# Performance work log

Hardware: AMD Instinct MI355X
Metric: run time of the kernel (lower is better)

## Reference

```python
import jax, jax.numpy as jnp
import numpy as np

N_NODES = 50000
N_EDGES = 800000
F = 64
R = 32


def setup_inputs() -> dict:
    key = jax.random.key(0)
    ks = jax.random.split(key, 12)
    s = jax.random.normal(ks[0], (N_NODES, F), dtype=jnp.float32)
    v = jax.random.normal(ks[1], (N_NODES, 3, F), dtype=jnp.float32)
    radial_embeddings = jax.random.normal(ks[2], (N_EDGES, R), dtype=jnp.float32)
    f_cut = jax.random.uniform(ks[3], (N_EDGES,), dtype=jnp.float32)
    unit_vectors = jax.random.normal(ks[4], (N_EDGES, 3), dtype=jnp.float32)
    edge_index = jax.random.randint(ks[5], (2, N_EDGES), 0, N_NODES, dtype=jnp.int64 if jax.config.jax_enable_x64 else jnp.int32)
    # mlp_phi: Linear(F,F) -> SiLU -> Linear(F, 3F); linear_W: Linear(R, 3F)
    W1 = jax.random.normal(ks[6], (F, F), dtype=jnp.float32) / np.sqrt(F)
    b1 = jnp.zeros((F,), dtype=jnp.float32)
    W2 = jax.random.normal(ks[7], (F, 3 * F), dtype=jnp.float32) / np.sqrt(F)
    b2 = jnp.zeros((3 * F,), dtype=jnp.float32)
    Wr = jax.random.normal(ks[8], (R, 3 * F), dtype=jnp.float32) / np.sqrt(R)
    br = jnp.zeros((3 * F,), dtype=jnp.float32)
    return {"s": s, "v": v, "radial_embeddings": radial_embeddings, "f_cut": f_cut,
            "unit_vectors": unit_vectors, "edge_index": edge_index,
            "W1": W1, "b1": b1, "W2": W2, "b2": b2, "Wr": Wr, "br": br}


def reference(s, v, radial_embeddings, f_cut, unit_vectors, edge_index, W1, b1, W2, b2, Wr, br):
    idx_i, idx_j = edge_index[0], edge_index[1]
    n_nodes = s.shape[0]
    nf = s.shape[-1]
    # per-node MLP: Linear -> SiLU -> Linear to 3F channels
    phi = jax.nn.silu(s @ W1 + b1) @ W2 + b2            # [N, 3F]
    # radial filter weighted by cutoff
    W = (radial_embeddings @ Wr + br) * f_cut[:, None]   # [E, 3F]
    x = phi[idx_j] * W                                   # [E, 3F]  (gather + multiply)
    x_s, x_vv, x_vs = x[:, :nf], x[:, nf:2 * nf], x[:, 2 * nf:]
    ds = jax.ops.segment_sum(x_s, idx_i, num_segments=n_nodes)          # [N, F]
    x_v = v[idx_j] * x_vv[:, None, :] + x_vs[:, None, :] * unit_vectors[:, :, None]  # [E, 3, F]
    dv = jax.ops.segment_sum(x_v, idx_i, num_segments=n_nodes)          # [N, 3, F]
    return s + ds, v + dv
```

## Files before the change

### kernel.cpp

```cpp
#include <hip/hip_runtime.h>
#include <math.h>

#define N_NODES 50000
#define N_EDGES 800000
#define F 64
#define R 32
#define C3F 192
#define CAP 48
#define CSTRIDE 16
#define MLP_BLOCKS ((N_NODES + 31) / 32)
#define FILL_BLOCKS ((N_EDGES + 1023) / 1024)

#define REP32(X) X(0) X(1) X(2) X(3) X(4) X(5) X(6) X(7) \
                 X(8) X(9) X(10) X(11) X(12) X(13) X(14) X(15) \
                 X(16) X(17) X(18) X(19) X(20) X(21) X(22) X(23) \
                 X(24) X(25) X(26) X(27) X(28) X(29) X(30) X(31)

__device__ __forceinline__ float bcastf(float x, int l) {
    return __uint_as_float((unsigned)__builtin_amdgcn_readlane(
        (int)__float_as_uint(x), l));
}

__global__ __launch_bounds__(256) void mlp_fill_kernel(
    const float* __restrict__ s, const float* __restrict__ W1,
    const float* __restrict__ b1, const float* __restrict__ W2,
    const float* __restrict__ b2, float* __restrict__ phi,
    const int* __restrict__ eidx, int* __restrict__ counts,
    int2* __restrict__ bucket)
{
    __shared__ float hid_s[32][68];

    if (blockIdx.x >= MLP_BLOCKS) {
        int base = (blockIdx.x - MLP_BLOCKS) * 1024 + threadIdx.x;
        int ii[4], jj[4];
#pragma unroll
        for (int q = 0; q < 4; q++) {
            int e = base + q * 256;
            ii[q] = -1;
            if (e < N_EDGES) {
                ii[q] = __builtin_nontemporal_load(&eidx[e]);
                jj[q] = __builtin_nontemporal_load(&eidx[N_EDGES + e]);
            }
        }
#pragma unroll
        for (int q = 0; q < 4; q++) {
            int e = base + q * 256;
            if (ii[q] >= 0) {
                int pos = atomicAdd(&counts[ii[q] * CSTRIDE], 1);
                if (pos < CAP)
                    bucket[(size_t)ii[q] * CAP + pos] = make_int2(e, jj[q]);
            }
        }
        return;
    }

    int n = threadIdx.x >> 3;
    int seg = threadIdx.x & 7;
    int node = blockIdx.x * 32 + n;
    bool live = node < N_NODES;

    if (live) {
        float sv[F];
        const float4* srow = (const float4*)(s + (size_t)node * F);
#pragma unroll
        for (int q = 0; q < F / 4; q++) {
            float4 t = srow[q];
            sv[4*q+0] = t.x; sv[4*q+1] = t.y; sv[4*q+2] = t.z; sv[4*q+3] = t.w;
        }
        float acc[8];
#pragma unroll
        for (int q = 0; q < 8; q++) acc[q] = b1[seg * 8 + q];
#pragma unroll
        for (int k = 0; k < F; k++) {
            float sk = sv[k];
            const float4* w = (const float4*)(W1 + (size_t)k * F + seg * 8);
            float4 w0 = w[0], w1 = w[1];
            acc[0] += sk * w0.x; acc[1] += sk * w0.y;
            acc[2] += sk * w0.z; acc[3] += sk * w0.w;
            acc[4] += sk * w1.x; acc[5] += sk * w1.y;
            acc[6] += sk * w1.z; acc[7] += sk * w1.w;
        }
#pragma unroll
        for (int q = 0; q < 8; q++) {
            float a = acc[q];
            hid_s[n][seg * 8 + q] = a / (1.f + __expf(-a));
        }
    }
    __syncthreads();

    if (!live) return;

    float hv[F];
#pragma unroll
    for (int q = 0; q < F; q++) hv[q] = hid_s[n][q];

    float acc[24];
#pragma unroll
    for (int q = 0; q < 24; q++) acc[q] = b2[seg * 24 + q];
#pragma unroll
    for (int k = 0; k < F; k++) {
        float hk = hv[k];
        const float4* w = (const float4*)(W2 + (size_t)k * C3F + seg * 24);
#pragma unroll
        for (int q4 = 0; q4 < 6; q4++) {
            float4 wv = w[q4];
            acc[q4*4+0] += hk * wv.x;
            acc[q4*4+1] += hk * wv.y;
            acc[q4*4+2] += hk * wv.z;
            acc[q4*4+3] += hk * wv.w;
        }
    }
    float4* o = (float4*)(phi + (size_t)node * C3F + seg * 24);
#pragma unroll
    for (int q4 = 0; q4 < 6; q4++)
        o[q4] = make_float4(acc[q4*4+0], acc[q4*4+1], acc[q4*4+2], acc[q4*4+3]);
}

__global__ __launch_bounds__(64, 3) void gather_kernel(
    const float* __restrict__ s, const float* __restrict__ v,
    const float* __restrict__ phi, const float* __restrict__ radial,
    const float* __restrict__ f_cut, const float* __restrict__ unit_vec,
    const float* __restrict__ Wr, const float* __restrict__ br,
    const int* __restrict__ counts, const int2* __restrict__ bucket,
    float* __restrict__ out_s, float* __restrict__ out_v)
{
    const int lane = threadIdx.x;
    const int node = blockIdx.x;

#define DECL_WR(r) float wrs##r, wrv##r, wrq##r;
    REP32(DECL_WR)
#undef DECL_WR
#define LOAD_WR(r) { const float* w_ = Wr + (r) * C3F; \
                     wrs##r = w_[lane]; wrv##r = w_[64 + lane]; \
                     wrq##r = w_[128 + lane]; }
    REP32(LOAD_WR)
#undef LOAD_WR

#define KA3(r) , "+v"(wrs##r), "+v"(wrv##r), "+v"(wrq##r)
#define PIN_WR \
    asm volatile("" : "+v"(wrs0) KA3(1) KA3(2) KA3(3) KA3(4) KA3(5) KA3(6) KA3(7), "+v"(wrv0), "+v"(wrq0)); \
    asm volatile("" : "+v"(wrs8) KA3(9) KA3(10) KA3(11) KA3(12) KA3(13) KA3(14) KA3(15), "+v"(wrv8), "+v"(wrq8)); \
    asm volatile("" : "+v"(wrs16) KA3(17) KA3(18) KA3(19) KA3(20) KA3(21) KA3(22) KA3(23), "+v"(wrv16), "+v"(wrq16)); \
    asm volatile("" : "+v"(wrs24) KA3(25) KA3(26) KA3(27) KA3(28) KA3(29) KA3(30) KA3(31), "+v"(wrv24), "+v"(wrq24));
    PIN_WR

    const float b_s = br[lane], b_vv = br[64 + lane], b_vs = br[128 + lane];

    float acc_s = 0.f, acc_v0 = 0.f, acc_v1 = 0.f, acc_v2 = 0.f;

    int cnt = __builtin_amdgcn_readfirstlane(counts[node * CSTRIDE]);
    cnt = cnt < CAP ? cnt : CAP;

    const int* rowi = (const int*)(bucket + (size_t)node * CAP);
    int ejx = 0, ejy = 0;
    if (lane < cnt) {
        ejx = __builtin_nontemporal_load(rowi + 2 * lane);
        ejy = __builtin_nontemporal_load(rowi + 2 * lane + 1);
    }
    float fcL = __builtin_nontemporal_load(&f_cut[ejx]);
    float u0L = __builtin_nontemporal_load(&unit_vec[ejx * 3 + 0]);
    float u1L = __builtin_nontemporal_load(&unit_vec[ejx * 3 + 1]);
    float u2L = __builtin_nontemporal_load(&unit_vec[ejx * 3 + 2]);

    if (cnt > 0) {
        int e = __builtin_amdgcn_readlane(ejx, 0);
        int j = __builtin_amdgcn_readlane(ejy, 0);
        const float* pj = phi + (size_t)j * C3F;
        const float* vj = v + (size_t)j * C3F;
        float ps = pj[lane], pvv = pj[64 + lane], pvs = pj[128 + lane];
        float va = vj[lane], vb = vj[64 + lane], vc = vj[128 + lane];
        float rl = __builtin_nontemporal_load(
            &radial[(size_t)(unsigned)e * R + (lane & 31)]);

        for (int k = 0; k < cnt; ++k) {
            int kn = (k + 1 < cnt) ? k + 1 : k;
            int j_n = __builtin_amdgcn_readlane(ejy, kn);
            int e_n = __builtin_amdgcn_readlane(ejx, kn);
            const float* pn = phi + (size_t)(unsigned)j_n * C3F;
            const float* vn = v + (size_t)(unsigned)j_n * C3F;
            float nps = pn[lane], npvv = pn[64 + lane], npvs = pn[128 + lane];
            float nva = vn[lane], nvb = vn[64 + lane], nvc = vn[128 + lane];
            float nrl = __builtin_nontemporal_load(
                &radial[(size_t)(unsigned)e_n * R + (lane & 31)]);

            float fc = bcastf(fcL, k);
            float u0 = bcastf(u0L, k);
            float u1 = bcastf(u1L, k);
            float u2 = bcastf(u2L, k);

            PIN_WR

            float ws = b_s, wvv = b_vv, wvs = b_vs;
#define FMA_WR(r) { float rr = bcastf(rl, r); ws += rr * wrs##r; \
                    wvv += rr * wrv##r; wvs += rr * wrq##r; }
            REP32(FMA_WR)
#undef FMA_WR

            float xs  = ps  * ws  * fc;
            float xvv = pvv * wvv * fc;
            float xvs = pvs * wvs * fc;
            acc_s  += xs;
            acc_v0 += va * xvv + xvs * u0;
            acc_v1 += vb * xvv + xvs * u1;
            acc_v2 += vc * xvv + xvs * u2;

            e = e_n; j = j_n;
            ps = nps; pvv = npvv; pvs = npvs;
            va = nva; vb = nvb; vc = nvc;
            rl = nrl;
        }
    }
#undef KA3
#undef PIN_WR

    float so = s[(size_t)node * F + lane] + acc_s;
    __builtin_nontemporal_store(so, &out_s[(size_t)node * F + lane]);
    const float* vi = v + (size_t)node * C3F;
    float* ovi = out_v + (size_t)node * C3F;
    __builtin_nontemporal_store(vi[lane]       + acc_v0, &ovi[lane]);
    __builtin_nontemporal_store(vi[64 + lane]  + acc_v1, &ovi[64 + lane]);
    __builtin_nontemporal_store(vi[128 + lane] + acc_v2, &ovi[128 + lane]);
}

extern "C" void kernel_launch(void* const* d_in, const int* in_sizes, int n_in,
                              void* d_out, int out_size, void* d_ws, size_t ws_size,
                              hipStream_t stream)
{
    const float* s      = (const float*)d_in[0];
    const float* v      = (const float*)d_in[1];
    const float* radial = (const float*)d_in[2];
    const float* f_cut  = (const float*)d_in[3];
    const float* unit   = (const float*)d_in[4];
    const int*   eidx   = (const int*)  d_in[5];
    const float* W1     = (const float*)d_in[6];
    const float* b1     = (const float*)d_in[7];
    const float* W2     = (const float*)d_in[8];
    const float* b2     = (const float*)d_in[9];
    const float* Wr     = (const float*)d_in[10];
    const float* br     = (const float*)d_in[11];

    float* out   = (float*)d_out;
    float* out_s = out;
    float* out_v = out + (size_t)N_NODES * F;

    float* phi    = (float*)d_ws;
    int*   counts = (int*)(phi + (size_t)N_NODES * C3F);
    int2*  bucket = (int2*)(counts + (size_t)N_NODES * CSTRIDE);

    hipMemsetAsync(counts, 0, (size_t)N_NODES * CSTRIDE * sizeof(int), stream);

    mlp_fill_kernel<<<MLP_BLOCKS + FILL_BLOCKS, 256, 0, stream>>>(
        s, W1, b1, W2, b2, phi, eidx, counts, bucket);

    gather_kernel<<<N_NODES, 64, 0, stream>>>(
        s, v, phi, radial, f_cut, unit, Wr, br,
        counts, bucket, out_s, out_v);
}
```

Measured before the change: 605.5 us.

## Double-buffer edge loads two ahead and use scalar radial loads

The gather loop now keeps two in-flight edge buffers (A/B), so phi, v and radial data are prefetched two edges ahead instead of one. Radial embeddings are read as 32 uniform scalar loads per edge instead of a per-lane load plus readlane broadcasts. The occupancy hint rises from 3 to 4 waves. The extra buffer adds about 38 live registers against the tighter launch bound, which could cause spills.

```diff
diff --git a/kernel.cpp b/kernel.cpp
--- a/kernel.cpp
+++ b/kernel.cpp
@@ -116,7 +116,7 @@
         o[q4] = make_float4(acc[q4*4+0], acc[q4*4+1], acc[q4*4+2], acc[q4*4+3]);
 }
 
-__global__ __launch_bounds__(64, 3) void gather_kernel(
+__global__ __launch_bounds__(64, 4) void gather_kernel(
     const float* __restrict__ s, const float* __restrict__ v,
     const float* __restrict__ phi, const float* __restrict__ radial,
     const float* __restrict__ f_cut, const float* __restrict__ unit_vec,
@@ -163,52 +163,81 @@
     float u2L = __builtin_nontemporal_load(&unit_vec[ejx * 3 + 2]);
 
     if (cnt > 0) {
-        int e = __builtin_amdgcn_readlane(ejx, 0);
-        int j = __builtin_amdgcn_readlane(ejy, 0);
-        const float* pj = phi + (size_t)j * C3F;
-        const float* vj = v + (size_t)j * C3F;
-        float ps = pj[lane], pvv = pj[64 + lane], pvs = pj[128 + lane];
-        float va = vj[lane], vb = vj[64 + lane], vc = vj[128 + lane];
-        float rl = __builtin_nontemporal_load(
-            &radial[(size_t)(unsigned)e * R + (lane & 31)]);
-
-        for (int k = 0; k < cnt; ++k) {
-            int kn = (k + 1 < cnt) ? k + 1 : k;
-            int j_n = __builtin_amdgcn_readlane(ejy, kn);
-            int e_n = __builtin_amdgcn_readlane(ejx, kn);
-            const float* pn = phi + (size_t)(unsigned)j_n * C3F;
-            const float* vn = v + (size_t)(unsigned)j_n * C3F;
-            float nps = pn[lane], npvv = pn[64 + lane], npvs = pn[128 + lane];
-            float nva = vn[lane], nvb = vn[64 + lane], nvc = vn[128 + lane];
-            float nrl = __builtin_nontemporal_load(
-                &radial[(size_t)(unsigned)e_n * R + (lane & 31)]);
-
-            float fc = bcastf(fcL, k);
-            float u0 = bcastf(u0L, k);
-            float u1 = bcastf(u1L, k);
-            float u2 = bcastf(u2L, k);
-
-            PIN_WR
-
-            float ws = b_s, wvv = b_vv, wvs = b_vs;
-#define FMA_WR(r) { float rr = bcastf(rl, r); ws += rr * wrs##r; \
-                    wvv += rr * wrv##r; wvs += rr * wrq##r; }
-            REP32(FMA_WR)
-#undef FMA_WR
-
-            float xs  = ps  * ws  * fc;
-            float xvv = pvv * wvv * fc;
-            float xvs = pvs * wvs * fc;
-            acc_s  += xs;
-            acc_v0 += va * xvv + xvs * u0;
-            acc_v1 += vb * xvv + xvs * u1;
-            acc_v2 += vc * xvv + xvs * u2;
-
-            e = e_n; j = j_n;
-            ps = nps; pvv = npvv; pvs = npvs;
-            va = nva; vb = nvb; vc = nvc;
-            rl = nrl;
-        }
+        float psA, pvvA, pvsA, vaA, vbA, vcA;
+        float psB = 0.f, pvvB = 0.f, pvsB = 0.f, vaB = 0.f, vbB = 0.f, vcB = 0.f;
+#define DECL_CR(r) float crA##r, crB##r = 0.f;
+        REP32(DECL_CR)
+#undef DECL_CR
+
+        {
+            int e0 = __builtin_amdgcn_readlane(ejx, 0);
+            int j0 = __builtin_amdgcn_readlane(ejy, 0);
+            const float* pj = phi + (size_t)(unsigned)j0 * C3F;
+            const float* vj = v + (size_t)(unsigned)j0 * C3F;
+            psA = pj[lane]; pvvA = pj[64 + lane]; pvsA = pj[128 + lane];
+            vaA = vj[lane]; vbA = vj[64 + lane]; vcA = vj[128 + lane];
+            const float* rp = radial + (size_t)(unsigned)e0 * R;
+#define LD_A(r) crA##r = rp[r];
+            REP32(LD_A)
+#undef LD_A
+        }
+        if (cnt > 1) {
+            int e1 = __builtin_amdgcn_readlane(ejx, 1);
+            int j1 = __builtin_amdgcn_readlane(ejy, 1);
+            const float* pj = phi + (size_t)(unsigned)j1 * C3F;
+            const float* vj = v + (size_t)(unsigned)j1 * C3F;
+            psB = pj[lane]; pvvB = pj[64 + lane]; pvsB = pj[128 + lane];
+            vaB = vj[lane]; vbB = vj[64 + lane]; vcB = vj[128 + lane];
+            const float* rp = radial + (size_t)(unsigned)e1 * R;
+#define LD_B(r) crB##r = rp[r];
+            REP32(LD_B)
+#undef LD_B
+        }
+
+#define CONSUME_REFILL(S, k, krefill)                                        \
+        {                                                                    \
+            float fc = bcastf(fcL, (k));                                     \
+            float u0 = bcastf(u0L, (k));                                     \
+            float u1 = bcastf(u1L, (k));                                     \
+            float u2 = bcastf(u2L, (k));                                     \
+            PIN_WR                                                           \
+            float ws = b_s, wvv = b_vv, wvs = b_vs;                          \
+            REP32(FMA_##S)                                                   \
+            float xs  = ps##S  * ws  * fc;                                   \
+            float xvv = pvv##S * wvv * fc;                                   \
+            float xvs = pvs##S * wvs * fc;                                   \
+            acc_s  += xs;                                                    \
+            acc_v0 += va##S * xvv + xvs * u0;                                \
+            acc_v1 += vb##S * xvv + xvs * u1;                                \
+            acc_v2 += vc##S * xvv + xvs * u2;                                \
+            if ((krefill) < cnt) {                                           \
+                int e_n = __builtin_amdgcn_readlane(ejx, (krefill));         \
+                int j_n = __builtin_amdgcn_readlane(ejy, (krefill));         \
+                const float* pn = phi + (size_t)(unsigned)j_n * C3F;         \
+                const float* vn = v + (size_t)(unsigned)j_n * C3F;           \
+                ps##S = pn[lane]; pvv##S = pn[64 + lane]; pvs##S = pn[128 + lane]; \
+                va##S = vn[lane]; vb##S = vn[64 + lane]; vc##S = vn[128 + lane];   \
+                const float* rp = radial + (size_t)(unsigned)e_n * R;        \
+                REP32(LDN_##S)                                               \
+            }                                                                \
+        }
+
+#define FMA_A(r) { ws += crA##r * wrs##r; wvv += crA##r * wrv##r; wvs += crA##r * wrq##r; }
+#define FMA_B(r) { ws += crB##r * wrs##r; wvv += crB##r * wrv##r; wvs += crB##r * wrq##r; }
+#define LDN_A(r) crA##r = rp[r];
+#define LDN_B(r) crB##r = rp[r];
+
+        for (int k = 0; k < cnt; k += 2) {
+            CONSUME_REFILL(A, k, k + 2)
+            if (k + 1 < cnt) {
+                CONSUME_REFILL(B, k + 1, k + 3)
+            }
+        }
+#undef FMA_A
+#undef FMA_B
+#undef LDN_A
+#undef LDN_B
+#undef CONSUME_REFILL
     }
 #undef KA3
 #undef PIN_WR
```

After: 1.070 ms. +76.7%, slower.
